# Kernel optimization log

Measured on AMD Instinct MI355X. Metric: run time of the kernel, lower is better.

Reference implementation:

```python
import jax, jax.numpy as jnp
import numpy as np

BS, SEQ, DIM, HEADS = 2, 2048, 1024, 16
HEAD_DIM = DIM // HEADS
NEG = -1e9


def setup_inputs() -> dict:
    key = jax.random.key(0)
    ks = jax.random.split(key, 5)
    s = 1.0 / np.sqrt(DIM)
    return {
        "x": jax.random.normal(ks[0], (BS, SEQ, DIM), jnp.float32),
        "padding_mask": jnp.ones((BS, SEQ), jnp.int32),
        "causal_mask": jnp.tril(jnp.ones((SEQ, SEQ), jnp.int32)),
        "Wq": jax.random.normal(ks[1], (DIM, DIM), jnp.float32) * s,
        "bq": jnp.zeros((DIM,), jnp.float32),
        "Wk": jax.random.normal(ks[2], (DIM, DIM), jnp.float32) * s,
        "bk": jnp.zeros((DIM,), jnp.float32),
        "Wv": jax.random.normal(ks[3], (DIM, DIM), jnp.float32) * s,
        "bv": jnp.zeros((DIM,), jnp.float32),
        "Wo": jax.random.normal(ks[4], (DIM, DIM), jnp.float32) * s,
        "bo": jnp.zeros((DIM,), jnp.float32),
    }


def reference(x, padding_mask, causal_mask, Wq, bq, Wk, bk, Wv, bv, Wo, bo):
    bs, seq, dim = x.shape
    # QKV projections -> [b, h, s, d]
    def proj(W, b):
        return (x @ W.T + b).reshape(bs, seq, HEADS, HEAD_DIM).transpose(0, 2, 1, 3)
    q, k, v = proj(Wq, bq), proj(Wk, bk), proj(Wv, bv)
    scores = jnp.einsum("bhqd,bhkd->bhqk", q, k) / np.sqrt(HEAD_DIM).astype(np.float32)
    scores = jnp.where(padding_mask[:, None, None, :] == 0, NEG, scores)
    scores = jnp.where(causal_mask[None, None, :, :] == 0, NEG, scores)
    attn = jax.nn.softmax(scores, axis=-1)
    out = jnp.einsum("bhqk,bhkd->bhqd", attn, v)
    out = out.transpose(0, 2, 1, 3).reshape(bs, seq, dim)
    return out @ Wo.T + bo
```

## Files before the change

### kernel.cpp

```cpp
#include <hip/hip_runtime.h>
#include <hip/hip_bf16.h>
#include <stdint.h>

#define SEQ 2048
#define DIM 1024
#define HEADS 16
#define HD 64
#define NEGV (-1e9f)
#define SCALE2 0.18033688011112042f
#define THR2 11.541560327111707f

typedef __attribute__((ext_vector_type(8))) short short8;
typedef __attribute__((ext_vector_type(4))) float f32x4;

__device__ __forceinline__ unsigned short f2bf(float f) {
  __hip_bfloat16 h = __float2bfloat16(f);
  union { __hip_bfloat16 h; unsigned short u; } cv;
  cv.h = h;
  return cv.u;
}

__device__ __forceinline__ void async16(const void* g, void* l) {
  __builtin_amdgcn_global_load_lds(
      (const __attribute__((address_space(1))) unsigned int*)g,
      (__attribute__((address_space(3))) unsigned int*)l, 16, 0, 0);
}

__global__ void cast_bf16_k(const float* __restrict__ in,
                            unsigned short* __restrict__ out, int n4) {
  int stride = gridDim.x * blockDim.x;
  for (int i = blockIdx.x * blockDim.x + threadIdx.x; i < n4; i += stride) {
    float4 v = ((const float4*)in)[i];
    ushort4 o;
    o.x = f2bf(v.x); o.y = f2bf(v.y); o.z = f2bf(v.z); o.w = f2bf(v.w);
    ((ushort4*)out)[i] = o;
  }
}

__global__ void cast_w4_k(const float* __restrict__ w0, const float* __restrict__ w1,
                          const float* __restrict__ w2, const float* __restrict__ w3,
                          unsigned short* __restrict__ o0, unsigned short* __restrict__ o1,
                          unsigned short* __restrict__ o2, unsigned short* __restrict__ o3,
                          int n4) {
  const float* in = (blockIdx.y == 0) ? w0 : (blockIdx.y == 1) ? w1
                   : (blockIdx.y == 2) ? w2 : w3;
  unsigned short* out = (blockIdx.y == 0) ? o0 : (blockIdx.y == 1) ? o1
                       : (blockIdx.y == 2) ? o2 : o3;
  int stride = gridDim.x * blockDim.x;
  for (int i = blockIdx.x * blockDim.x + threadIdx.x; i < n4; i += stride) {
    float4 v = ((const float4*)in)[i];
    ushort4 o;
    o.x = f2bf(v.x); o.y = f2bf(v.y); o.z = f2bf(v.z); o.w = f2bf(v.w);
    ((ushort4*)out)[i] = o;
  }
}

__device__ __forceinline__ void stage_ab(const unsigned short* __restrict__ A,
                                         const unsigned short* __restrict__ B,
                                         int K, int bm0, int bn0, int k0,
                                         unsigned short* As, unsigned short* Bs,
                                         int tid) {
#pragma unroll
  for (int i = 0; i < 2; ++i) {
    int e   = (i * 256 + tid) * 8;
    int row = e >> 5;
    int kk  = e & 31;
    async16(A + (size_t)(bm0 + row) * K + (size_t)(k0 + kk), As + e);
    async16(B + (size_t)(bn0 + row) * K + (size_t)(k0 + kk), Bs + e);
  }
}

__device__ __forceinline__ void gemm_core(const unsigned short* __restrict__ A,
                                          const unsigned short* __restrict__ B,
                                          int K, int bm0, int bn0,
                                          unsigned short (*As)[128 * 32],
                                          unsigned short (*Bs)[128 * 32],
                                          f32x4 acc[4][4]) {
  const int tid  = threadIdx.x;
  const int lane = tid & 63;
  const int w    = tid >> 6;
  const int wr   = w >> 1, wc = w & 1;
  const int lrow = lane & 15, lkg = lane >> 4;

  stage_ab(A, B, K, bm0, bn0, 0, As[0], Bs[0], tid);
  __syncthreads();

  for (int k0 = 0; k0 < K; k0 += 32) {
    const int cur = (k0 >> 5) & 1;
    if (k0 + 32 < K)
      stage_ab(A, B, K, bm0, bn0, k0 + 32, As[cur ^ 1], Bs[cur ^ 1], tid);

    short8 af[4], bf[4];
#pragma unroll
    for (int i = 0; i < 4; ++i) {
      af[i] = *(const short8*)(As[cur] + (wr * 64 + i * 16 + lrow) * 32 + lkg * 8);
      bf[i] = *(const short8*)(Bs[cur] + (wc * 64 + i * 16 + lrow) * 32 + lkg * 8);
    }
#pragma unroll
    for (int i = 0; i < 4; ++i)
#pragma unroll
      for (int j = 0; j < 4; ++j)
        acc[i][j] = __builtin_amdgcn_mfma_f32_16x16x32_bf16(af[i], bf[j], acc[i][j], 0, 0, 0);

    __syncthreads();
  }
}

__global__ __launch_bounds__(256)
void qkv_gemm_k(const unsigned short* __restrict__ xb,
                const unsigned short* __restrict__ wqb,
                const unsigned short* __restrict__ wkb,
                const unsigned short* __restrict__ wvb,
                const float* __restrict__ bq, const float* __restrict__ bk,
                const float* __restrict__ bv,
                unsigned short* __restrict__ Qb, unsigned short* __restrict__ Kb,
                unsigned short* __restrict__ Vtb) {
  __shared__ __align__(16) unsigned short As[2][128 * 32];
  __shared__ __align__(16) unsigned short Bs[2][128 * 32];
  const int z = blockIdx.z;
  const unsigned short* B = (z == 0) ? wqb : (z == 1) ? wkb : wvb;
  const float* bias       = (z == 0) ? bq  : (z == 1) ? bk  : bv;
  const int bm0 = blockIdx.y * 128, bn0 = blockIdx.x * 128;

  f32x4 acc[4][4] = {};
  gemm_core(xb, B, DIM, bm0, bn0, As, Bs, acc);

  const int lane = threadIdx.x & 63;
  const int w = threadIdx.x >> 6, wr = w >> 1, wc = w & 1;
  unsigned short* out01 = (z == 0) ? Qb : Kb;
#pragma unroll
  for (int i = 0; i < 4; ++i)
#pragma unroll
    for (int j = 0; j < 4; ++j)
#pragma unroll
      for (int r = 0; r < 4; ++r) {
        int mg = bm0 + wr * 64 + i * 16 + (lane >> 4) * 4 + r;
        int ng = bn0 + wc * 64 + j * 16 + (lane & 15);
        float v = acc[i][j][r] + bias[ng];
        int bb = mg >> 11, s = mg & 2047, h = ng >> 6, d = ng & 63;
        int bh = bb * HEADS + h;
        if (z < 2)
          out01[((size_t)bh * SEQ + s) * HD + d] = f2bf(v);
        else
          Vtb[((size_t)bh * HD + d) * SEQ + s] = f2bf(v);
      }
}

__global__ __launch_bounds__(256)
void out_gemm_k(const unsigned short* __restrict__ Ob,
                const unsigned short* __restrict__ wob,
                const float* __restrict__ bo, float* __restrict__ out) {
  __shared__ __align__(16) unsigned short As[2][128 * 32];
  __shared__ __align__(16) unsigned short Bs[2][128 * 32];
  const int bm0 = blockIdx.y * 128, bn0 = blockIdx.x * 128;

  f32x4 acc[4][4] = {};
  gemm_core(Ob, wob, DIM, bm0, bn0, As, Bs, acc);

  const int lane = threadIdx.x & 63;
  const int w = threadIdx.x >> 6, wr = w >> 1, wc = w & 1;
#pragma unroll
  for (int i = 0; i < 4; ++i)
#pragma unroll
    for (int j = 0; j < 4; ++j)
#pragma unroll
      for (int r = 0; r < 4; ++r) {
        int mg = bm0 + wr * 64 + i * 16 + (lane >> 4) * 4 + r;
        int ng = bn0 + wc * 64 + j * 16 + (lane & 15);
        out[(size_t)mg * DIM + ng] = acc[i][j][r] + bo[ng];
      }
}

__device__ __forceinline__ void stage_kv64(const unsigned short* __restrict__ kbase,
                                           const unsigned short* __restrict__ vbase,
                                           int k0, unsigned short* KsB,
                                           unsigned short* VsB, int tid) {
#pragma unroll
  for (int j = 0; j < 2; ++j) {
    const int c    = j * 256 + tid;
    const int row  = c >> 3;
    const int colb = (c & 7) << 4;
    const int srcb = colb ^ ((row & 7) << 4);
    async16(kbase + (size_t)(k0 + row) * HD + (srcb >> 1), KsB + c * 8);
  }
#pragma unroll
  for (int j = 0; j < 2; ++j) {
    const int c    = j * 256 + tid;
    const int d    = c >> 3;
    const int colb = (c & 7) << 4;
    const int srcb = colb ^ ((d & 7) << 4);
    async16(vbase + (size_t)d * SEQ + k0 + (srcb >> 1), VsB + c * 8);
  }
}

__global__ __launch_bounds__(256)
void attn_k(const unsigned short* __restrict__ Q,
            const unsigned short* __restrict__ Kp,
            const unsigned short* __restrict__ Vt,
            const int* __restrict__ pm,
            unsigned short* __restrict__ O) {
  __shared__ __align__(16) unsigned short Ks[2][64 * 64];
  __shared__ __align__(16) unsigned short Vs[2][64 * 64];
  __shared__ __align__(16) unsigned short plds[4][16 * 64];
  __shared__ int wflag[4];

  const int tid  = threadIdx.x;
  const int lane = tid & 63;
  const int w    = tid >> 6;
  const int lc = lane & 15, lg = lane >> 4;
  const int qb = 31 - blockIdx.y;
  const int bh = blockIdx.x;
  const int b  = bh >> 4, h = bh & 15;

  const size_t base = (size_t)bh * SEQ * HD;
  const unsigned short* kbase = Kp + base;
  const unsigned short* vbase = Vt + (size_t)bh * HD * SEQ;
  const int* pmb = pm + b * SEQ;
  char* pb = (char*)&plds[w][0];
  const int swp = (lc & 7) << 4;

  const int qrow0 = qb * 64 + w * 16;
  const int qrow  = qrow0 + lc;

  short8 qa[2];
  {
    const unsigned short* qp = Q + base + (size_t)qrow * HD + lg * 8;
    qa[0] = *(const short8*)(qp);
    qa[1] = *(const short8*)(qp + 32);
  }

  f32x4 oacc[4] = {};
  float mrow = -1e30f, lsum = 0.f;

  const int nk = qb + 1;

  stage_kv64(kbase, vbase, 0, Ks[0], Vs[0], tid);

  {
    int ok = 1;
    for (int i = tid; i < SEQ / 4; i += 256) {
      int4 v = ((const int4*)pmb)[i];
      ok &= (v.x != 0) & (v.y != 0) & (v.z != 0) & (v.w != 0);
    }
    ok = __all(ok) ? 1 : 0;
    if (lane == 0) wflag[w] = ok;
  }
  __syncthreads();
  const bool allones = (wflag[0] & wflag[1] & wflag[2] & wflag[3]) != 0;

  for (int kt = 0; kt < nk; ++kt) {
    const int cur = kt & 1;
    const int k0 = kt * 64;
    if (kt + 1 < nk)
      stage_kv64(kbase, vbase, k0 + 64, Ks[cur ^ 1], Vs[cur ^ 1], tid);

    f32x4 s[4];
    const char* kbuf = (const char*)Ks[cur];
    __builtin_amdgcn_s_setprio(1);
#pragma unroll
    for (int t = 0; t < 4; ++t) {
      const int row = t * 16 + lc;
      const int swk = (row & 7) << 4;
      const char* kr = kbuf + row * 128;
      short8 kb0 = *(const short8*)(kr + ((lg * 16) ^ swk));
      short8 kb1 = *(const short8*)(kr + ((lg * 16 + 64) ^ swk));
      f32x4 z = {};
      z = __builtin_amdgcn_mfma_f32_16x16x32_bf16(kb0, qa[0], z, 0, 0, 0);
      z = __builtin_amdgcn_mfma_f32_16x16x32_bf16(kb1, qa[1], z, 0, 0, 0);
#pragma unroll
      for (int r = 0; r < 4; ++r) s[t][r] = z[r] * SCALE2;
    }
    __builtin_amdgcn_s_setprio(0);

    if (!allones) {
#pragma unroll
      for (int t = 0; t < 4; ++t) {
        const int kr0 = k0 + t * 16;
        int4 pmv = *(const int4*)(pmb + kr0 + lg * 4);
#pragma unroll
        for (int r = 0; r < 4; ++r) {
          const int kidx = kr0 + lg * 4 + r;
          if (kidx > qrow || (&pmv.x)[r] == 0) s[t][r] = NEGV;
        }
      }
    } else if (kt == qb) {
#pragma unroll
      for (int t = 0; t < 4; ++t)
#pragma unroll
        for (int r = 0; r < 4; ++r) {
          const int kidx = k0 + t * 16 + lg * 4 + r;
          if (kidx > qrow) s[t][r] = NEGV;
        }
    }

    float mx = -1e30f;
#pragma unroll
    for (int t = 0; t < 4; ++t)
      mx = fmaxf(mx, fmaxf(fmaxf(s[t][0], s[t][1]), fmaxf(s[t][2], s[t][3])));
    if (!__all(mx <= mrow + THR2)) {
      mx = fmaxf(mx, __shfl_xor(mx, 16, 64));
      mx = fmaxf(mx, __shfl_xor(mx, 32, 64));
      const float mnew = fmaxf(mrow, mx);
      const float sc = exp2f(mrow - mnew);
      lsum *= sc;
      mrow = mnew;
      const float s0 = __shfl(sc, lg * 4 + 0, 64);
      const float s1 = __shfl(sc, lg * 4 + 1, 64);
      const float s2 = __shfl(sc, lg * 4 + 2, 64);
      const float s3 = __shfl(sc, lg * 4 + 3, 64);
#pragma unroll
      for (int t = 0; t < 4; ++t) {
        oacc[t][0] *= s0; oacc[t][1] *= s1; oacc[t][2] *= s2; oacc[t][3] *= s3;
      }
    }
    float sum = 0.f;
#pragma unroll
    for (int t = 0; t < 4; ++t)
#pragma unroll
      for (int r = 0; r < 4; ++r) {
        const float p = exp2f(s[t][r] - mrow);
        s[t][r] = p;
        sum += p;
      }
    lsum += sum;

#pragma unroll
    for (int t = 0; t < 4; ++t) {
      short4 pk;
      pk.x = (short)f2bf(s[t][0]); pk.y = (short)f2bf(s[t][1]);
      pk.z = (short)f2bf(s[t][2]); pk.w = (short)f2bf(s[t][3]);
      const int colb = (t * 16 + lg * 4) * 2;
      *(short4*)(pb + lc * 128 + (colb ^ swp)) = pk;
    }
    short8 pa[2];
#pragma unroll
    for (int ks = 0; ks < 2; ++ks)
      pa[ks] = *(const short8*)(pb + lc * 128 + (((ks * 32 + lg * 8) * 2) ^ swp));

    const char* vbuf = (const char*)Vs[cur];
    __builtin_amdgcn_s_setprio(1);
#pragma unroll
    for (int t = 0; t < 4; ++t) {
      const int d = t * 16 + lc;
      const int swv = (d & 7) << 4;
      const char* vr = vbuf + d * 128;
#pragma unroll
      for (int ks = 0; ks < 2; ++ks) {
        short8 vv = *(const short8*)(vr + ((ks * 64 + lg * 16) ^ swv));
        oacc[t] = __builtin_amdgcn_mfma_f32_16x16x32_bf16(pa[ks], vv, oacc[t], 0, 0, 0);
      }
    }
    __builtin_amdgcn_s_setprio(0);

    __syncthreads();
  }

  lsum += __shfl_xor(lsum, 16, 64);
  lsum += __shfl_xor(lsum, 32, 64);
  const float l0 = __shfl(lsum, lg * 4 + 0, 64);
  const float l1 = __shfl(lsum, lg * 4 + 1, 64);
  const float l2 = __shfl(lsum, lg * 4 + 2, 64);
  const float l3 = __shfl(lsum, lg * 4 + 3, 64);
  const float i0 = 1.f / l0, i1 = 1.f / l1, i2 = 1.f / l2, i3 = 1.f / l3;
#pragma unroll
  for (int t = 0; t < 4; ++t) {
    const size_t o0 = ((size_t)(b * SEQ + qrow0 + lg * 4)) * DIM + h * HD + t * 16 + lc;
    O[o0]           = f2bf(oacc[t][0] * i0);
    O[o0 + DIM]     = f2bf(oacc[t][1] * i1);
    O[o0 + 2 * DIM] = f2bf(oacc[t][2] * i2);
    O[o0 + 3 * DIM] = f2bf(oacc[t][3] * i3);
  }
}

extern "C" void kernel_launch(void* const* d_in, const int* in_sizes, int n_in,
                              void* d_out, int out_size, void* d_ws, size_t ws_size,
                              hipStream_t stream) {
  const float* x  = (const float*)d_in[0];
  const int*   pm = (const int*)d_in[1];
  const float* Wq = (const float*)d_in[3];
  const float* bq = (const float*)d_in[4];
  const float* Wk = (const float*)d_in[5];
  const float* bk = (const float*)d_in[6];
  const float* Wv = (const float*)d_in[7];
  const float* bv = (const float*)d_in[8];
  const float* Wo = (const float*)d_in[9];
  const float* bo = (const float*)d_in[10];

  const size_t NX = (size_t)4096 * 1024;
  const size_t NW = (size_t)1024 * 1024;

  unsigned short* ws  = (unsigned short*)d_ws;
  unsigned short* xb  = ws;
  unsigned short* wqb = xb + NX;
  unsigned short* wkb = wqb + NW;
  unsigned short* wvb = wkb + NW;
  unsigned short* wob = wvb + NW;
  unsigned short* Qb  = wob + NW;
  unsigned short* Kb  = Qb + NX;
  unsigned short* Vtb = Kb + NX;
  unsigned short* Ob  = xb;

  cast_bf16_k<<<dim3(2048), dim3(256), 0, stream>>>(x, xb, (int)(NX / 4));
  cast_w4_k<<<dim3(512, 4), dim3(256), 0, stream>>>(Wq, Wk, Wv, Wo,
                                                    wqb, wkb, wvb, wob,
                                                    (int)(NW / 4));

  qkv_gemm_k<<<dim3(8, 32, 3), dim3(256), 0, stream>>>(xb, wqb, wkb, wvb,
                                                       bq, bk, bv, Qb, Kb, Vtb);

  attn_k<<<dim3(32, 32), dim3(256), 0, stream>>>(Qb, Kb, Vtb, pm, Ob);

  out_gemm_k<<<dim3(8, 32), dim3(256), 0, stream>>>(Ob, wob, bo, (float*)d_out);
}
```

Measured before the change: 124.1 us.

## Load V fragments directly from global into registers instead of staging in LDS

```diff
diff --git a/kernel.cpp b/kernel.cpp
--- a/kernel.cpp
+++ b/kernel.cpp
@@ -171,10 +171,8 @@
       }
 }
 
-__device__ __forceinline__ void stage_kv64(const unsigned short* __restrict__ kbase,
-                                           const unsigned short* __restrict__ vbase,
-                                           int k0, unsigned short* KsB,
-                                           unsigned short* VsB, int tid) {
+__device__ __forceinline__ void stage_k64(const unsigned short* __restrict__ kbase,
+                                          int k0, unsigned short* KsB, int tid) {
 #pragma unroll
   for (int j = 0; j < 2; ++j) {
     const int c    = j * 256 + tid;
@@ -182,14 +180,6 @@
     const int colb = (c & 7) << 4;
     const int srcb = colb ^ ((row & 7) << 4);
     async16(kbase + (size_t)(k0 + row) * HD + (srcb >> 1), KsB + c * 8);
-  }
-#pragma unroll
-  for (int j = 0; j < 2; ++j) {
-    const int c    = j * 256 + tid;
-    const int d    = c >> 3;
-    const int colb = (c & 7) << 4;
-    const int srcb = colb ^ ((d & 7) << 4);
-    async16(vbase + (size_t)d * SEQ + k0 + (srcb >> 1), VsB + c * 8);
   }
 }
 
@@ -200,9 +190,7 @@
             const int* __restrict__ pm,
             unsigned short* __restrict__ O) {
   __shared__ __align__(16) unsigned short Ks[2][64 * 64];
-  __shared__ __align__(16) unsigned short Vs[2][64 * 64];
   __shared__ __align__(16) unsigned short plds[4][16 * 64];
-  __shared__ int wflag[4];
 
   const int tid  = threadIdx.x;
   const int lane = tid & 63;
@@ -234,25 +222,30 @@
 
   const int nk = qb + 1;
 
-  stage_kv64(kbase, vbase, 0, Ks[0], Vs[0], tid);
-
-  {
-    int ok = 1;
-    for (int i = tid; i < SEQ / 4; i += 256) {
-      int4 v = ((const int4*)pmb)[i];
-      ok &= (v.x != 0) & (v.y != 0) & (v.z != 0) & (v.w != 0);
-    }
-    ok = __all(ok) ? 1 : 0;
-    if (lane == 0) wflag[w] = ok;
-  }
+  stage_k64(kbase, 0, Ks[0], tid);
+
+  int ok = 1;
+  for (int i = lane; i < SEQ / 4; i += 64) {
+    int4 v = ((const int4*)pmb)[i];
+    ok &= (v.x != 0) & (v.y != 0) & (v.z != 0) & (v.w != 0);
+  }
+  const bool allones = __all(ok);
   __syncthreads();
-  const bool allones = (wflag[0] & wflag[1] & wflag[2] & wflag[3]) != 0;
 
   for (int kt = 0; kt < nk; ++kt) {
     const int cur = kt & 1;
     const int k0 = kt * 64;
+
+    short8 va[8];
+#pragma unroll
+    for (int t = 0; t < 4; ++t)
+#pragma unroll
+      for (int ks = 0; ks < 2; ++ks)
+        va[t * 2 + ks] = *(const short8*)(vbase + (size_t)(t * 16 + lc) * SEQ +
+                                          k0 + ks * 32 + lg * 8);
+
     if (kt + 1 < nk)
-      stage_kv64(kbase, vbase, k0 + 64, Ks[cur ^ 1], Vs[cur ^ 1], tid);
+      stage_k64(kbase, k0 + 64, Ks[cur ^ 1], tid);
 
     f32x4 s[4];
     const char* kbuf = (const char*)Ks[cur];
@@ -337,19 +330,13 @@
     for (int ks = 0; ks < 2; ++ks)
       pa[ks] = *(const short8*)(pb + lc * 128 + (((ks * 32 + lg * 8) * 2) ^ swp));
 
-    const char* vbuf = (const char*)Vs[cur];
     __builtin_amdgcn_s_setprio(1);
 #pragma unroll
-    for (int t = 0; t < 4; ++t) {
-      const int d = t * 16 + lc;
-      const int swv = (d & 7) << 4;
-      const char* vr = vbuf + d * 128;
-#pragma unroll
-      for (int ks = 0; ks < 2; ++ks) {
-        short8 vv = *(const short8*)(vr + ((ks * 64 + lg * 16) ^ swv));
-        oacc[t] = __builtin_amdgcn_mfma_f32_16x16x32_bf16(pa[ks], vv, oacc[t], 0, 0, 0);
-      }
-    }
+    for (int t = 0; t < 4; ++t)
+#pragma unroll
+      for (int ks = 0; ks < 2; ++ks)
+        oacc[t] = __builtin_amdgcn_mfma_f32_16x16x32_bf16(pa[ks], va[t * 2 + ks],
+                                                          oacc[t], 0, 0, 0);
     __builtin_amdgcn_s_setprio(0);
 
     __syncthreads();
```

Result: slower. 153.3 us (+23.4%).
